# Kernel optimization log

Measured on AMD Instinct MI355X. Metric: run time of the kernel, lower is better.

The kernel has to match this reference:

```python
import jax, jax.numpy as jnp
import numpy as np

N = 50000          # nodes
E = 1_600_000      # edges (before self-loops)
F_IN = 512         # feature_num
H1, C1 = 8, 8      # conv1: heads=8, out_channels=8
OUT = 128          # output_num (conv2, heads=1)
NEG_SLOPE = 0.2    # GATConv default leaky-relu slope


def gat_conv(x, W, a_src, a_dst, bias, src, dst, heads, ch, concat):
    """PyG GATConv (eval mode) on edge list (src -> dst)."""
    n = x.shape[0]
    h = (x @ W).reshape(n, heads, ch)                      # [N,H,C]
    alpha_src = (h * a_src).sum(-1)                        # [N,H]
    alpha_dst = (h * a_dst).sum(-1)                        # [N,H]
    e = alpha_src[src] + alpha_dst[dst]                    # [E,H]
    e = jnp.where(e > 0, e, NEG_SLOPE * e)                 # leaky_relu
    # segment softmax over edges sharing the same destination
    e_max = jax.ops.segment_max(e, dst, num_segments=n)    # self-loops => no empty segs
    w = jnp.exp(e - e_max[dst])
    denom = jax.ops.segment_sum(w, dst, num_segments=n)
    alpha = w / denom[dst]                                 # [E,H]
    msg = h[src] * alpha[:, :, None]                       # [E,H,C]
    out = jax.ops.segment_sum(msg, dst, num_segments=n)    # [N,H,C]
    out = out.reshape(n, heads * ch) if concat else out.mean(axis=1)
    return out + bias


def setup_inputs() -> dict:
    key = jax.random.key(0)
    ks = jax.random.split(key, 10)
    x = jax.random.normal(ks[0], (N, F_IN), dtype=jnp.float32)
    edge_index = jax.random.randint(ks[1], (2, E), 0, N, dtype=jnp.int64)
    s = 0.1
    return {
        "x": x,
        "edge_index": edge_index,
        "W1": jax.random.normal(ks[2], (F_IN, H1 * C1), dtype=jnp.float32) * s,
        "att_src1": jax.random.normal(ks[3], (H1, C1), dtype=jnp.float32) * s,
        "att_dst1": jax.random.normal(ks[4], (H1, C1), dtype=jnp.float32) * s,
        "b1": jnp.zeros((H1 * C1,), dtype=jnp.float32),
        "W2": jax.random.normal(ks[5], (H1 * C1, OUT), dtype=jnp.float32) * s,
        "att_src2": jax.random.normal(ks[6], (1, OUT), dtype=jnp.float32) * s,
        "att_dst2": jax.random.normal(ks[7], (1, OUT), dtype=jnp.float32) * s,
        "b2": jnp.zeros((OUT,), dtype=jnp.float32),
    }


def reference(x, edge_index, W1, att_src1, att_dst1, b1, W2, att_src2, att_dst2, b2):
    # PyG GATConv adds self-loops by default
    loops = jnp.arange(N, dtype=edge_index.dtype)
    src = jnp.concatenate([edge_index[0], loops])
    dst = jnp.concatenate([edge_index[1], loops])
    h = gat_conv(x, W1, att_src1, att_dst1, b1, src, dst, H1, C1, concat=True)
    h = jax.nn.elu(h)
    out = gat_conv(h, W2, att_src2, att_dst2, b2, src, dst, 1, OUT, concat=False)
    return out
```

## Files before the change

kernel.cpp:

```cpp
#include <hip/hip_runtime.h>
#include <math.h>

#define N_NODES 50000
#define F_IN    512
#define H1      8
#define C1      8
#define D1      64
#define OUT_C   128
#define NEG     0.2f

#define SCHUNK  256
#define SNBLK   ((N_NODES + SCHUNK - 1)/SCHUNK)

#define NHB      256
#define HTHREADS 1024
#define HW8      ((N_NODES + 3)/4)

#define G1_ROWS  224
#define G1_THR   896
#define NB1      ((N_NODES + G1_ROWS - 1)/G1_ROWS)

using bf16x8 = __attribute__((ext_vector_type(8))) short;
using f32x4  = __attribute__((ext_vector_type(4))) float;
typedef unsigned short u16;
typedef unsigned int   u32;
typedef unsigned char  u8;

__device__ __forceinline__ float leaky(float x){
    return fmaxf(x, 0.f) + NEG * fminf(x, 0.f);
}
__device__ __forceinline__ u16 f2bf(float f){
    u32 u = __float_as_uint(f);
    u32 r = u + 0x7FFF + ((u>>16)&1);
    return (u16)(r>>16);
}
__device__ __forceinline__ float bf2f(u16 h){ return __uint_as_float(((u32)h)<<16); }

__device__ __forceinline__ void cvt8(const float4& a, const float4& b, bf16x8& hi, bf16x8& lo){
    u16 h0=f2bf(a.x),h1=f2bf(a.y),h2=f2bf(a.z),h3=f2bf(a.w);
    u16 h4=f2bf(b.x),h5=f2bf(b.y),h6=f2bf(b.z),h7=f2bf(b.w);
    hi = (bf16x8){(short)h0,(short)h1,(short)h2,(short)h3,
                  (short)h4,(short)h5,(short)h6,(short)h7};
    lo = (bf16x8){(short)f2bf(a.x-bf2f(h0)),(short)f2bf(a.y-bf2f(h1)),
                  (short)f2bf(a.z-bf2f(h2)),(short)f2bf(a.w-bf2f(h3)),
                  (short)f2bf(b.x-bf2f(h4)),(short)f2bf(b.y-bf2f(h5)),
                  (short)f2bf(b.z-bf2f(h6)),(short)f2bf(b.w-bf2f(h7))};
}

__global__ __launch_bounds__(1024) void k_histB(const int* __restrict__ dst_a, int E, int CE,
                                                u8* __restrict__ histmat){
    __shared__ u32 lcnt[HW8];
    const int blk = blockIdx.x;
    const int i0 = blk*CE;
    const int i1 = min(i0+CE, E + N_NODES);
    for (int w=threadIdx.x; w<HW8; w+=HTHREADS) lcnt[w]=0;
    __syncthreads();
    for (int i=i0+(int)threadIdx.x; i<i1; i+=HTHREADS){
        int d = (i<E)? dst_a[i] : (i-E);
        atomicAdd(&lcnt[d>>2], 1u<<((d&3)*8));
    }
    __syncthreads();
    u32* dst = (u32*)(histmat + (size_t)blk*N_NODES);
    for (int w=threadIdx.x; w<HW8; w+=HTHREADS) dst[w] = lcnt[w];
}

__global__ __launch_bounds__(256) void k_colscan(u8* __restrict__ histmat, int* __restrict__ cnt,
                                                 int* __restrict__ bsum){
    __shared__ int sm[256];
    int n = blockIdx.x*256 + threadIdx.x;
    u32 run = 0;
    if (n < N_NODES){
        u8* p = histmat + n;
        #pragma unroll 4
        for (int b=0;b<NHB;b++){
            u32 v = p[(size_t)b*N_NODES];
            p[(size_t)b*N_NODES] = (u8)run;
            run += v;
        }
        cnt[n] = (int)run;
    }
    sm[threadIdx.x] = (n < N_NODES) ? (int)run : 0;
    __syncthreads();
    for (int off=128; off>0; off>>=1){
        if (threadIdx.x < off) sm[threadIdx.x] += sm[threadIdx.x+off];
        __syncthreads();
    }
    if (threadIdx.x==0) bsum[blockIdx.x] = sm[0];
}

__global__ __launch_bounds__(256) void k_scanC2(const int* __restrict__ cnt, const int* __restrict__ bsum,
                                                int* __restrict__ rowptr,
                                                const float* __restrict__ W1, const float* __restrict__ W2,
                                                u16* __restrict__ whiT, u16* __restrict__ wloT,
                                                u16* __restrict__ w2hiT, u16* __restrict__ w2loT){
    __shared__ int sm[256];
    __shared__ int base;
    const int t = threadIdx.x;
    int v = (t < SNBLK) ? bsum[t] : 0;
    sm[t] = v; __syncthreads();
    for (int off=1; off<256; off<<=1){
        int u = (t>=off)? sm[t-off] : 0;
        __syncthreads();
        sm[t]+=u; __syncthreads();
    }
    if (t==0) base = (blockIdx.x==0) ? 0 : sm[blockIdx.x-1];
    if (blockIdx.x==0 && t==255) rowptr[N_NODES] = sm[SNBLK-1];
    __syncthreads();
    const int myoff = base;
    int idx = blockIdx.x*256 + t;
    int c = (idx<N_NODES)? cnt[idx] : 0;
    __syncthreads();
    sm[t]=c; __syncthreads();
    for (int off=1; off<256; off<<=1){
        int u = (t>=off)? sm[t-off] : 0;
        __syncthreads();
        sm[t]+=u; __syncthreads();
    }
    if (idx<N_NODES) rowptr[idx] = myoff + sm[t] - c;
    int gid = blockIdx.x*256 + t;
    if (gid < F_IN*D1){
        int k = gid >> 6, col = gid & 63;
        float w = W1[gid];
        u16 hi = f2bf(w);
        whiT[col*F_IN + k] = hi;
        wloT[col*F_IN + k] = f2bf(w - bf2f(hi));
    }
    if (gid < D1*OUT_C){
        int k = gid >> 7, col = gid & 127;
        float w = W2[gid];
        u16 hi = f2bf(w);
        w2hiT[col*D1 + k] = hi;
        w2loT[col*D1 + k] = f2bf(w - bf2f(hi));
    }
}

__global__ __launch_bounds__(1024) void k_scatterB(const int* __restrict__ src_a, const int* __restrict__ dst_a,
                                                   int E, int CE,
                                                   const u8* __restrict__ histmat, const int* __restrict__ rowptr,
                                                   u16* __restrict__ srcs){
    __shared__ u32 lcnt[HW8];
    const int blk = blockIdx.x;
    const int i0 = blk*CE;
    const int i1 = min(i0+CE, E + N_NODES);
    const u8* __restrict__ pb = histmat + (size_t)blk*N_NODES;
    for (int w=threadIdx.x; w<HW8; w+=HTHREADS) lcnt[w]=0;
    __syncthreads();
    for (int i=i0+(int)threadIdx.x; i<i1; i+=HTHREADS){
        int s, d;
        if (i<E){ s=src_a[i]; d=dst_a[i]; } else { s=d=i-E; }
        u32 old = atomicAdd(&lcnt[d>>2], 1u<<((d&3)*8));
        u32 rank = (old >> ((d&3)*8)) & 0xFFu;
        int pos = rowptr[d] + (int)pb[d] + (int)rank;
        srcs[pos] = (u16)s;
    }
}

__global__ __launch_bounds__(G1_THR) void k_gemm1(
        const float* __restrict__ x,
        const u16* __restrict__ whiT, const u16* __restrict__ wloT,
        const float* __restrict__ att_src, const float* __restrict__ att_dst,
        u16* __restrict__ h1b, float* __restrict__ asrc, float* __restrict__ adst){
    __shared__ u16 Bh[D1*F_IN];
    __shared__ u16 Bl[D1*F_IN];
    const int tid = threadIdx.x;
    const int wid = tid>>6, l = tid&63;
    const int lq = l>>4, lr = l&15;

    for (int i = tid; i < (D1*F_IN)/8; i += G1_THR){
        int col = i >> 6;
        int c   = i & 63;
        int boff = (col*1024 + c*16) ^ ((col&7)<<4);
        *(uint4*)((char*)Bh + boff) = *(const uint4*)(whiT + (size_t)i*8);
        *(uint4*)((char*)Bl + boff) = *(const uint4*)(wloT + (size_t)i*8);
    }
    __syncthreads();

    const int wavebase = blockIdx.x*G1_ROWS + wid*16;
    const int arow = min(wavebase + lr, N_NODES-1);
    const float* __restrict__ xrow = x + (size_t)arow*F_IN + lq*8;

    f32x4 acc[4];
    #pragma unroll
    for (int n=0;n<4;n++) acc[n] = (f32x4){0.f,0.f,0.f,0.f};

    float4 p0 = *(const float4*)(xrow);
    float4 p1 = *(const float4*)(xrow+4);
    float4 p2 = *(const float4*)(xrow+32);
    float4 p3 = *(const float4*)(xrow+36);

    for (int ks=0; ks<8; ks++){
        bf16x8 ahi0, alo0, ahi1, alo1;
        cvt8(p0, p1, ahi0, alo0);
        cvt8(p2, p3, ahi1, alo1);
        if (ks < 7){
            const float* nx = xrow + (ks+1)*64;
            p0 = *(const float4*)(nx);
            p1 = *(const float4*)(nx+4);
            p2 = *(const float4*)(nx+32);
            p3 = *(const float4*)(nx+36);
        }
        const int k0 = ks*64;
        #pragma unroll
        for (int n=0;n<4;n++){
            const int colb = n*16 + lr;
            const int swz  = (colb&7)<<4;
            const int b0 = (colb*1024 + (k0 + lq*8)*2) ^ swz;
            const int b1 = (colb*1024 + (k0 + 32 + lq*8)*2) ^ swz;
            bf16x8 bhi0 = *(const bf16x8*)((const char*)Bh + b0);
            bf16x8 blo0 = *(const bf16x8*)((const char*)Bl + b0);
            acc[n] = __builtin_amdgcn_mfma_f32_16x16x32_bf16(ahi0, bhi0, acc[n], 0,0,0);
            acc[n] = __builtin_amdgcn_mfma_f32_16x16x32_bf16(ahi0, blo0, acc[n], 0,0,0);
            acc[n] = __builtin_amdgcn_mfma_f32_16x16x32_bf16(alo0, bhi0, acc[n], 0,0,0);
            bf16x8 bhi1 = *(const bf16x8*)((const char*)Bh + b1);
            bf16x8 blo1 = *(const bf16x8*)((const char*)Bl + b1);
            acc[n] = __builtin_amdgcn_mfma_f32_16x16x32_bf16(ahi1, bhi1, acc[n], 0,0,0);
            acc[n] = __builtin_amdgcn_mfma_f32_16x16x32_bf16(ahi1, blo1, acc[n], 0,0,0);
            acc[n] = __builtin_amdgcn_mfma_f32_16x16x32_bf16(alo1, bhi1, acc[n], 0,0,0);
        }
    }

    #pragma unroll
    for (int n=0;n<4;n++){
        int col = n*16 + lr;
        float as_w = att_src[col], ad_w = att_dst[col];
        #pragma unroll
        for (int i=0;i<4;i++){
            int node = wavebase + lq*4 + i;
            float v = acc[n][i];
            float s = v*as_w, d = v*ad_w;
            s += __shfl_xor(s,1); d += __shfl_xor(d,1);
            s += __shfl_xor(s,2); d += __shfl_xor(d,2);
            s += __shfl_xor(s,4); d += __shfl_xor(d,4);
            if (node < N_NODES){
                h1b[(size_t)node*D1 + col] = f2bf(v);
                if ((l&7)==0){
                    int head = col>>3;
                    asrc[node*H1 + head] = s;
                    adst[node*H1 + head] = d;
                }
            }
        }
    }
}

__global__ __launch_bounds__(256) void k_agg1(
        const int* __restrict__ rowptr, const u16* __restrict__ srcs,
        const float* __restrict__ asrc1, const float* __restrict__ adst1,
        const u16* __restrict__ h1b, float* __restrict__ out1){
    const int node = blockIdx.x*4 + (threadIdx.x>>6);
    const int lane = threadIdx.x & 63;
    const int g = lane >> 3;
    const int p = lane & 7;
    const int r0 = __builtin_amdgcn_readfirstlane(rowptr[node]);
    const int r1 = __builtin_amdgcn_readfirstlane(rowptr[node+1]);
    const float ad = adst1[node*H1 + p];
    float a0=0,a1=0,a2=0,a3=0,a4=0,a5=0,a6=0,a7=0, den=0;
    for (int base=r0; base<r1; base+=64){
        int eidx = base + lane;
        int sl = srcs[eidx < r1 ? eidx : (r1-1)];
        const int m = min(64, r1-base);
        for (int k=0; k*8 < m; k++){
            int e = k*8 + g;
            int s = __shfl(sl, e);
            float w = (base + e < r1) ? __expf(leaky(asrc1[s*H1 + p] + ad)) : 0.f;
            uint4 pv = *(const uint4*)(h1b + (size_t)s*D1 + p*8);
            a0 += w*bf2f((u16)(pv.x&0xFFFFu)); a1 += w*bf2f((u16)(pv.x>>16));
            a2 += w*bf2f((u16)(pv.y&0xFFFFu)); a3 += w*bf2f((u16)(pv.y>>16));
            a4 += w*bf2f((u16)(pv.z&0xFFFFu)); a5 += w*bf2f((u16)(pv.z>>16));
            a6 += w*bf2f((u16)(pv.w&0xFFFFu)); a7 += w*bf2f((u16)(pv.w>>16));
            den += w;
        }
    }
    #pragma unroll
    for (int off=8; off<64; off<<=1){
        a0 += __shfl_xor(a0,off); a1 += __shfl_xor(a1,off);
        a2 += __shfl_xor(a2,off); a3 += __shfl_xor(a3,off);
        a4 += __shfl_xor(a4,off); a5 += __shfl_xor(a5,off);
        a6 += __shfl_xor(a6,off); a7 += __shfl_xor(a7,off);
        den += __shfl_xor(den,off);
    }
    if (g == 0){
        float inv = 1.f/den;
        float* o = out1 + (size_t)node*D1 + p*8;
        *(float4*)(o)   = make_float4(a0*inv, a1*inv, a2*inv, a3*inv);
        *(float4*)(o+4) = make_float4(a4*inv, a5*inv, a6*inv, a7*inv);
    }
}

__global__ __launch_bounds__(256) void k_gemm2(
        const float* __restrict__ out1, const float* __restrict__ b1,
        const u16* __restrict__ w2hiT, const u16* __restrict__ w2loT,
        const float* __restrict__ att_src2, const float* __restrict__ att_dst2,
        u16* __restrict__ h2b, float* __restrict__ asrc2, float* __restrict__ adst2){
    __shared__ u16 Ahi[64*64];
    __shared__ u16 Alo[64*64];
    const int tid = threadIdx.x;
    const int wid = tid>>6, l = tid&63;
    const int lq = l>>4, lr = l&15;
    const int rowbase = blockIdx.x*64;

    #pragma unroll
    for (int q=0;q<4;q++){
        int p = tid + 256*q;
        int r = p>>4, kseg = p&15;
        int grow = min(rowbase + r, N_NODES-1);
        float4 v = *(const float4*)(out1 + (size_t)grow*D1 + kseg*4);
        float4 bb = *(const float4*)(b1 + kseg*4);
        float a0 = v.x+bb.x, a1 = v.y+bb.y, a2 = v.z+bb.z, a3 = v.w+bb.w;
        a0 = a0>0.f ? a0 : (__expf(a0)-1.f);
        a1 = a1>0.f ? a1 : (__expf(a1)-1.f);
        a2 = a2>0.f ? a2 : (__expf(a2)-1.f);
        a3 = a3>0.f ? a3 : (__expf(a3)-1.f);
        u16 h0=f2bf(a0), h1v=f2bf(a1), h2v=f2bf(a2), h3v=f2bf(a3);
        u16 e0=f2bf(a0-bf2f(h0)), e1=f2bf(a1-bf2f(h1v)),
            e2=f2bf(a2-bf2f(h2v)), e3=f2bf(a3-bf2f(h3v));
        int boff = (r*128 + kseg*8) ^ ((r&7)<<4);
        *(ushort4*)((char*)Ahi + boff) = make_ushort4(h0,h1v,h2v,h3v);
        *(ushort4*)((char*)Alo + boff) = make_ushort4(e0,e1,e2,e3);
    }
    __syncthreads();

    const int arow = wid*16 + lr;
    bf16x8 ahi[2], alo[2];
    #pragma unroll
    for (int kt=0;kt<2;kt++){
        int boff = (arow*128 + kt*64 + lq*16) ^ ((arow&7)<<4);
        ahi[kt] = *(const bf16x8*)((const char*)Ahi + boff);
        alo[kt] = *(const bf16x8*)((const char*)Alo + boff);
    }

    f32x4 acc[8];
    #pragma unroll
    for (int n=0;n<8;n++) acc[n] = (f32x4){0.f,0.f,0.f,0.f};
    #pragma unroll
    for (int n=0;n<8;n++){
        #pragma unroll
        for (int kt=0;kt<2;kt++){
            const size_t wo = (size_t)(n*16+lr)*D1 + kt*32 + lq*8;
            bf16x8 bhi = *(const bf16x8*)(w2hiT + wo);
            bf16x8 blo = *(const bf16x8*)(w2loT + wo);
            acc[n] = __builtin_amdgcn_mfma_f32_16x16x32_bf16(ahi[kt], bhi, acc[n], 0,0,0);
            acc[n] = __builtin_amdgcn_mfma_f32_16x16x32_bf16(ahi[kt], blo, acc[n], 0,0,0);
            acc[n] = __builtin_amdgcn_mfma_f32_16x16x32_bf16(alo[kt], bhi, acc[n], 0,0,0);
        }
    }

    float aw[8], dw[8];
    #pragma unroll
    for (int n=0;n<8;n++){ aw[n]=att_src2[n*16+lr]; dw[n]=att_dst2[n*16+lr]; }
    #pragma unroll
    for (int i=0;i<4;i++){
        int node = rowbase + wid*16 + lq*4 + i;
        bool ok = node < N_NODES;
        float s = 0.f, d = 0.f;
        #pragma unroll
        for (int n=0;n<8;n++){
            float v = acc[n][i];
            s = fmaf(v, aw[n], s);
            d = fmaf(v, dw[n], d);
            if (ok) h2b[(size_t)node*OUT_C + n*16 + lr] = f2bf(v);
        }
        s += __shfl_xor(s,1); d += __shfl_xor(d,1);
        s += __shfl_xor(s,2); d += __shfl_xor(d,2);
        s += __shfl_xor(s,4); d += __shfl_xor(d,4);
        s += __shfl_xor(s,8); d += __shfl_xor(d,8);
        if (ok && lr==0){ asrc2[node]=s; adst2[node]=d; }
    }
}

__global__ __launch_bounds__(256) void k_agg2(
        const int* __restrict__ rowptr, const u16* __restrict__ srcs,
        const float* __restrict__ asrc2, const float* __restrict__ adst2,
        const u16* __restrict__ h2b, const float* __restrict__ b2,
        float* __restrict__ out){
    const int node = blockIdx.x*4 + (threadIdx.x>>6);
    const int lane = threadIdx.x & 63;
    const int g = lane >> 4;
    const int p = lane & 15;
    const int r0 = __builtin_amdgcn_readfirstlane(rowptr[node]);
    const int r1 = __builtin_amdgcn_readfirstlane(rowptr[node+1]);
    const float ad = adst2[node];
    float a0=0,a1=0,a2=0,a3=0,a4=0,a5=0,a6=0,a7=0, den=0;
    for (int base=r0; base<r1; base+=64){
        int eidx = base + lane;
        int sl = srcs[eidx < r1 ? eidx : (r1-1)];
        float wl = (eidx < r1) ? __expf(leaky(asrc2[sl] + ad)) : 0.f;
        const int m = min(64, r1-base);
        for (int k=0; k*4 < m; k++){
            int e = k*4 + g;
            int   s = __shfl(sl, e);
            float w = __shfl(wl, e);
            uint4 pv = *(const uint4*)(h2b + (size_t)s*OUT_C + p*8);
            a0 += w*bf2f((u16)(pv.x&0xFFFFu)); a1 += w*bf2f((u16)(pv.x>>16));
            a2 += w*bf2f((u16)(pv.y&0xFFFFu)); a3 += w*bf2f((u16)(pv.y>>16));
            a4 += w*bf2f((u16)(pv.z&0xFFFFu)); a5 += w*bf2f((u16)(pv.z>>16));
            a6 += w*bf2f((u16)(pv.w&0xFFFFu)); a7 += w*bf2f((u16)(pv.w>>16));
            den += w;
        }
    }
    #pragma unroll
    for (int off=16; off<64; off<<=1){
        a0 += __shfl_xor(a0,off); a1 += __shfl_xor(a1,off);
        a2 += __shfl_xor(a2,off); a3 += __shfl_xor(a3,off);
        a4 += __shfl_xor(a4,off); a5 += __shfl_xor(a5,off);
        a6 += __shfl_xor(a6,off); a7 += __shfl_xor(a7,off);
        den += __shfl_xor(den,off);
    }
    if (g == 0){
        float inv = 1.f/den;
        const float* bb = b2 + p*8;
        float* o = out + (size_t)node*OUT_C + p*8;
        *(float4*)(o)   = make_float4(a0*inv+bb[0], a1*inv+bb[1], a2*inv+bb[2], a3*inv+bb[3]);
        *(float4*)(o+4) = make_float4(a4*inv+bb[4], a5*inv+bb[5], a6*inv+bb[6], a7*inv+bb[7]);
    }
}

extern "C" void kernel_launch(void* const* d_in, const int* in_sizes, int n_in,
                              void* d_out, int out_size, void* d_ws, size_t ws_size,
                              hipStream_t stream) {
    const float* x        = (const float*)d_in[0];
    const int*   edge     = (const int*)  d_in[1];
    const float* W1       = (const float*)d_in[2];
    const float* att_src1 = (const float*)d_in[3];
    const float* att_dst1 = (const float*)d_in[4];
    const float* b1       = (const float*)d_in[5];
    const float* W2       = (const float*)d_in[6];
    const float* att_src2 = (const float*)d_in[7];
    const float* att_dst2 = (const float*)d_in[8];
    const float* b2       = (const float*)d_in[9];
    float* out = (float*)d_out;

    const int E  = in_sizes[1] / 2;
    const int ET = E + N_NODES;
    const int CE = (ET + NHB - 1) / NHB;
    const int* src_a = edge;
    const int* dst_a = edge + E;

    float* ws = (float*)d_ws;
    float* h1f   = ws;
    float* asrc1 = h1f   + (size_t)N_NODES*D1;
    float* adst1 = asrc1 + (size_t)N_NODES*H1;
    float* out1  = adst1 + (size_t)N_NODES*H1;
    float* h2f   = out1  + (size_t)N_NODES*D1;
    float* asrc2 = h2f   + (size_t)N_NODES*OUT_C;
    float* adst2 = asrc2 + N_NODES;
    int*   cnt    = (int*)(adst2 + N_NODES);
    int*   rowptr = cnt    + N_NODES;
    u16*   srcs   = (u16*)(rowptr + (N_NODES+4));
    int*   bsum   = (int*)(srcs + ((ET+3)&~3));
    u8*    histmat= (u8*)(bsum + 256);
    u16*   whiT   = (u16*)(histmat + (size_t)NHB*N_NODES);
    u16*   wloT   = whiT + F_IN*D1;
    u16*   w2hiT  = wloT + F_IN*D1;
    u16*   w2loT  = w2hiT + D1*OUT_C;
    u16*   h1b    = (u16*)h1f;
    u16*   h2b    = (u16*)h2f;

    hipLaunchKernelGGL(k_histB,   dim3(NHB), dim3(HTHREADS), 0, stream, dst_a, E, CE, histmat);
    hipLaunchKernelGGL(k_colscan, dim3(SNBLK), dim3(256), 0, stream, histmat, cnt, bsum);
    hipLaunchKernelGGL(k_scanC2,  dim3(SNBLK), dim3(256), 0, stream, cnt, bsum, rowptr,
                       W1, W2, whiT, wloT, w2hiT, w2loT);
    hipLaunchKernelGGL(k_scatterB,dim3(NHB), dim3(HTHREADS), 0, stream,
                       src_a, dst_a, E, CE, histmat, rowptr, srcs);

    hipLaunchKernelGGL(k_gemm1, dim3(NB1), dim3(G1_THR), 0, stream,
                       x, whiT, wloT, att_src1, att_dst1, h1b, asrc1, adst1);
    hipLaunchKernelGGL(k_agg1, dim3((N_NODES+3)/4), dim3(256), 0, stream,
                       rowptr, srcs, asrc1, adst1, h1b, out1);

    hipLaunchKernelGGL(k_gemm2, dim3((N_NODES+63)/64), dim3(256), 0, stream,
                       out1, b1, w2hiT, w2loT, att_src2, att_dst2, h2b, asrc2, adst2);
    hipLaunchKernelGGL(k_agg2, dim3((N_NODES+3)/4), dim3(256), 0, stream,
                       rowptr, srcs, asrc2, adst2, h2b, b2, out);
}
```

Measured before the change: 207.8 us.

## Record per-edge ranks in histogram pass and scatter edges with a flat grid

The histogram kernel now stores each edge's intra-block rank, taken from the shared-memory atomic's return value, into a byte array. The scatter kernel drops its 256-block LDS histogram replay and becomes a flat one-thread-per-edge kernel that reads that rank plus the block's column offset. This removes the second round of LDS atomics and the per-block LDS clearing, and it exposes far more parallelism than 256 blocks. In exchange it adds a byte write and a byte read per edge, plus scattered byte reads from the large histogram matrix.

Result: no change. 211.9 us (+2.0%).

```diff
diff --git a/kernel.cpp b/kernel.cpp
--- a/kernel.cpp
+++ b/kernel.cpp
@@ -48,7 +48,7 @@
 }
 
 __global__ __launch_bounds__(1024) void k_histB(const int* __restrict__ dst_a, int E, int CE,
-                                                u8* __restrict__ histmat){
+                                                u8* __restrict__ histmat, u8* __restrict__ ranks){
     __shared__ u32 lcnt[HW8];
     const int blk = blockIdx.x;
     const int i0 = blk*CE;
@@ -57,7 +57,8 @@
     __syncthreads();
     for (int i=i0+(int)threadIdx.x; i<i1; i+=HTHREADS){
         int d = (i<E)? dst_a[i] : (i-E);
-        atomicAdd(&lcnt[d>>2], 1u<<((d&3)*8));
+        u32 old = atomicAdd(&lcnt[d>>2], 1u<<((d&3)*8));
+        ranks[i] = (u8)((old >> ((d&3)*8)) & 0xFFu);
     }
     __syncthreads();
     u32* dst = (u32*)(histmat + (size_t)blk*N_NODES);
@@ -134,25 +135,19 @@
     }
 }
 
-__global__ __launch_bounds__(1024) void k_scatterB(const int* __restrict__ src_a, const int* __restrict__ dst_a,
-                                                   int E, int CE,
-                                                   const u8* __restrict__ histmat, const int* __restrict__ rowptr,
-                                                   u16* __restrict__ srcs){
-    __shared__ u32 lcnt[HW8];
-    const int blk = blockIdx.x;
-    const int i0 = blk*CE;
-    const int i1 = min(i0+CE, E + N_NODES);
-    const u8* __restrict__ pb = histmat + (size_t)blk*N_NODES;
-    for (int w=threadIdx.x; w<HW8; w+=HTHREADS) lcnt[w]=0;
-    __syncthreads();
-    for (int i=i0+(int)threadIdx.x; i<i1; i+=HTHREADS){
-        int s, d;
-        if (i<E){ s=src_a[i]; d=dst_a[i]; } else { s=d=i-E; }
-        u32 old = atomicAdd(&lcnt[d>>2], 1u<<((d&3)*8));
-        u32 rank = (old >> ((d&3)*8)) & 0xFFu;
-        int pos = rowptr[d] + (int)pb[d] + (int)rank;
-        srcs[pos] = (u16)s;
-    }
+__global__ __launch_bounds__(256) void k_scatterC(const int* __restrict__ src_a, const int* __restrict__ dst_a,
+                                                  int E, int CE,
+                                                  const u8* __restrict__ histmat, const u8* __restrict__ ranks,
+                                                  const int* __restrict__ rowptr,
+                                                  u16* __restrict__ srcs){
+    int i = blockIdx.x*blockDim.x + threadIdx.x;
+    int ET = E + N_NODES;
+    if (i >= ET) return;
+    int s, d;
+    if (i < E){ s = src_a[i]; d = dst_a[i]; } else { s = d = i - E; }
+    int blk = i / CE;
+    int pos = rowptr[d] + (int)histmat[(size_t)blk*N_NODES + d] + (int)ranks[i];
+    srcs[pos] = (u16)s;
 }
 
 __global__ __launch_bounds__(G1_THR) void k_gemm1(
@@ -448,7 +443,8 @@
     int*   rowptr = cnt    + N_NODES;
     u16*   srcs   = (u16*)(rowptr + (N_NODES+4));
     int*   bsum   = (int*)(srcs + ((ET+3)&~3));
-    u8*    histmat= (u8*)(bsum + 256);
+    u8*    ranks  = (u8*)(bsum + 256);
+    u8*    histmat= ranks + (((size_t)ET+15)&~15ull);
     u16*   whiT   = (u16*)(histmat + (size_t)NHB*N_NODES);
     u16*   wloT   = whiT + F_IN*D1;
     u16*   w2hiT  = wloT + F_IN*D1;
@@ -456,12 +452,12 @@
     u16*   h1b    = (u16*)h1f;
     u16*   h2b    = (u16*)h2f;
 
-    hipLaunchKernelGGL(k_histB,   dim3(NHB), dim3(HTHREADS), 0, stream, dst_a, E, CE, histmat);
+    hipLaunchKernelGGL(k_histB,   dim3(NHB), dim3(HTHREADS), 0, stream, dst_a, E, CE, histmat, ranks);
     hipLaunchKernelGGL(k_colscan, dim3(SNBLK), dim3(256), 0, stream, histmat, cnt, bsum);
     hipLaunchKernelGGL(k_scanC2,  dim3(SNBLK), dim3(256), 0, stream, cnt, bsum, rowptr,
                        W1, W2, whiT, wloT, w2hiT, w2loT);
-    hipLaunchKernelGGL(k_scatterB,dim3(NHB), dim3(HTHREADS), 0, stream,
-                       src_a, dst_a, E, CE, histmat, rowptr, srcs);
+    hipLaunchKernelGGL(k_scatterC,dim3((ET+255)/256), dim3(256), 0, stream,
+                       src_a, dst_a, E, CE, histmat, ranks, rowptr, srcs);
 
     hipLaunchKernelGGL(k_gemm1, dim3(NB1), dim3(G1_THR), 0, stream,
                        x, whiT, wloT, att_src1, att_dst1, h1b, asrc1, adst1);
```
